# Kernel tuning notes

Measured on AMD Instinct MI355X. Metric: run time of the kernel, lower is better.

Reference implementation:

```python
import jax, jax.numpy as jnp
import numpy as np

B, S, H, HEAD = 4, 4096, 512, 128
GAMMA = 0.96875
SCALE_BASE = 512  # XPOS default scale_base


def rotate_every_two(x):
    # (..., d) -> interleave (-x2, x1) pairs, matching torch stack+flatten
    x1 = x[..., ::2]
    x2 = x[..., 1::2]
    return jnp.stack((-x2, x1), axis=-1).reshape(x.shape)


def duplicate_interleave(m):
    # (L, d/2) -> (L, d): each column repeated twice, interleaved
    return jnp.repeat(m, 2, axis=-1)


def xpos(x, downscale=False):
    # x: (B, L, d). Faithful to XPOS module with offset=0.
    L, d = x.shape[1], x.shape[2]
    half = d // 2
    base_scale = (jnp.arange(0, d, 2, dtype=jnp.float32) + 0.4 * d) / (1.4 * d)  # (half,)
    power = jnp.arange(L, dtype=jnp.float32)[:, None] / SCALE_BASE              # (L,1)
    scale = base_scale[None, :] ** power                                        # (L,half)
    inv_freq = 1.0 / (10000.0 ** (jnp.arange(half, dtype=jnp.float32) / half))  # (half,)
    sinusoid = jnp.arange(L, dtype=jnp.float32)[:, None] * inv_freq[None, :]    # (L,half)
    sin, cos = jnp.sin(sinusoid), jnp.cos(sinusoid)
    if downscale:
        scale = 1.0 / scale
    sin = duplicate_interleave(sin * scale)  # (L,d)
    cos = duplicate_interleave(cos * scale)  # (L,d)
    return x * cos[None] + rotate_every_two(x) * sin[None]


def decay_mask(s1, s2, gamma):
    n = jnp.arange(s1)[:, None]
    m = jnp.arange(s2)[None, :]
    keep = n >= m
    # guard exponent to avoid inf for n<m (original zeroes NaNs from inf*0)
    exp = jnp.where(keep, (n - m).astype(jnp.float32), 0.0)
    return jnp.where(keep, gamma ** exp, 0.0)  # (s1,s2)


def setup_inputs() -> dict:
    key = jax.random.key(0)
    k1, k2, k3, k4, k5 = jax.random.split(key, 5)
    return {
        "X": jax.random.normal(k1, (B, S, H), dtype=jnp.float32),
        "Mem": jax.random.normal(k2, (B, S, H), dtype=jnp.float32),
        "W_Q": jax.random.normal(k3, (H, HEAD), dtype=jnp.float32) / H,
        "W_K": jax.random.normal(k4, (H, HEAD), dtype=jnp.float32) / H,
        "W_V": jax.random.normal(k5, (H, HEAD), dtype=jnp.float32) / H,
    }


def reference(X, Mem, W_Q, W_K, W_V):
    s1, s2 = X.shape[1], Mem.shape[1]
    D = decay_mask(s1, s2, GAMMA)                 # (s1,s2)
    Q = xpos(X @ W_Q)                              # (B,s1,head)
    K = xpos(Mem @ W_K, downscale=True)            # (B,s2,head)
    V = Mem @ W_V                                  # (B,s2,v)
    ret = jnp.einsum("bnd,bmd->bnm", Q, K) * D[None]  # (B,s1,s2)
    return ret @ V                                 # (B,s1,v)
```

## Files before the change

### kernel.cpp

```cpp
#include <hip/hip_runtime.h>
#include <hip/hip_bf16.h>

#define S_LEN 4096
#define HID   512
#define HD    128
#define LOG2_GAMMA (-0.0458036933f)

typedef short bf16x8 __attribute__((ext_vector_type(8)));
typedef float f32x4  __attribute__((ext_vector_type(4)));
typedef unsigned short u16;

static __device__ __forceinline__ u16 f2bf(float f) {
    union { float f; unsigned u; } v; v.f = f;
    unsigned r = (v.u + 0x7fffu + ((v.u >> 16) & 1u)) >> 16;
    return (u16)r;
}

static __device__ __forceinline__ unsigned pk2(float lo, float hi) {
    __hip_bfloat162 h = __float22bfloat162_rn(make_float2(lo, hi));
    union { __hip_bfloat162 h; unsigned u; } c; c.h = h; return c.u;
}
static __device__ __forceinline__ bf16x8 pack8(float4 a, float4 b) {
    union { unsigned u[4]; bf16x8 v; } r;
    r.u[0] = pk2(a.x, a.y); r.u[1] = pk2(a.z, a.w);
    r.u[2] = pk2(b.x, b.y); r.u[3] = pk2(b.z, b.w);
    return r.v;
}

static __device__ __forceinline__ void gload16(const void* g, void* l) {
    __builtin_amdgcn_global_load_lds(
        (const __attribute__((address_space(1))) unsigned*)g,
        (__attribute__((address_space(3))) unsigned*)l, 16, 0, 0);
}

__global__ __launch_bounds__(256) void xpos_table_kernel(float2* __restrict__ tabQ,
                                                         float2* __restrict__ tabK) {
    int idx = blockIdx.x * 256 + threadIdx.x;
    int n = idx >> 6, i = idx & 63;
    float base  = (2.0f * i + 51.2f) * (1.0f / 179.2f);
    float power = (float)n * (1.0f / 512.0f);
    float scale = exp2f(power * log2f(base));
    float inv_freq = exp2f(-(float)i * (13.287712379549449f / 64.0f));
    float theta = (float)n * inv_freq;
    float s, c;
    sincosf(theta, &s, &c);
    tabQ[idx] = make_float2(c * scale, s * scale);
    float is = 1.0f / scale;
    tabK[idx] = make_float2(c * is, s * is);
}

__global__ __launch_bounds__(256) void wt_kernel(const float* __restrict__ WQ,
                                                 const float* __restrict__ WK,
                                                 const float* __restrict__ WV,
                                                 u16* __restrict__ Wt) {
    int idx = blockIdx.x * 256 + threadIdx.x;
    int w = idx >> 16;
    int rem = idx & 65535;
    int c = rem >> 9, k = rem & 511;
    const float* src = (w == 0) ? WQ : (w == 1) ? WK : WV;
    Wt[idx] = f2bf(src[k * HD + c]);
}

__global__ __launch_bounds__(256) void proj_kernel(const float* __restrict__ X,
                                                   const float* __restrict__ Mem,
                                                   const u16* __restrict__ Wt,
                                                   const float2* __restrict__ tabQ,
                                                   const float2* __restrict__ tabK,
                                                   u16* __restrict__ Qo,
                                                   u16* __restrict__ Ko,
                                                   u16* __restrict__ Vt) {
    __shared__ __align__(16) float A_lds[2][4096];
    __shared__ __align__(16) u16   B_lds[2][8192];
    const int which = blockIdx.y;
    const int tid  = threadIdx.x;
    const int wave = tid >> 6, lane = tid & 63;
    const int l15  = lane & 15, quad = lane >> 4;
    const int rt_base = blockIdx.x * 64;
    const float* src = (which == 0) ? X : Mem;
    const u16*  Wsel = Wt + which * 65536;

    auto stage = [&](int ch, int p) {
        const int kc0 = ch * 64;
#pragma unroll
        for (int i = 0; i < 4; ++i) {
            int u = i * 256 + tid;
            int row = u >> 4;
            int s = (u & 15) ^ (row & 15);
            gload16(src + (size_t)(rt_base + row) * HID + kc0 + s * 4,
                    &A_lds[p][(i * 256 + wave * 64) * 4]);
        }
#pragma unroll
        for (int i = 0; i < 4; ++i) {
            int u = i * 256 + tid;
            int col = u >> 3;
            int s = (u & 7) ^ (col & 7);
            gload16(Wsel + (size_t)col * HID + kc0 + s * 8,
                    &B_lds[p][(i * 256 + wave * 64) * 8]);
        }
    };

    f32x4 acc[8];
#pragma unroll
    for (int ct = 0; ct < 8; ++ct) acc[ct] = (f32x4){0.f, 0.f, 0.f, 0.f};

    stage(0, 0);
    for (int ch = 0; ch < 8; ++ch) {
        const int p = ch & 1;
        __syncthreads();
        if (ch < 7) stage(ch + 1, p ^ 1);
#pragma unroll
        for (int kc2 = 0; kc2 < 2; ++kc2) {
            const int s0 = kc2 * 8 + quad * 2;
            const int arow = wave * 16 + l15;
            float4 af0 = *(const float4*)&A_lds[p][(arow * 16 + ((s0    ) ^ l15)) * 4];
            float4 af1 = *(const float4*)&A_lds[p][(arow * 16 + ((s0 + 1) ^ l15)) * 4];
            bf16x8 a = pack8(af0, af1);
#pragma unroll
            for (int ct = 0; ct < 8; ++ct) {
                const int col = ct * 16 + l15;
                const int sb = (kc2 * 4 + quad) ^ (col & 7);
                bf16x8 bf = *(const bf16x8*)&B_lds[p][(col * 8 + sb) * 8];
                acc[ct] = __builtin_amdgcn_mfma_f32_16x16x32_bf16(a, bf, acc[ct], 0, 0, 0);
            }
        }
    }

    if (which <= 1) {
        const float2* tab = (which == 0) ? tabQ : tabK;
        u16* outp = (which == 0) ? Qo : Ko;
#pragma unroll
        for (int ct = 0; ct < 8; ++ct) {
            int j = ct * 16 + l15;
            int i = j >> 1;
            float sgn = (j & 1) ? 1.0f : -1.0f;
#pragma unroll
            for (int r = 0; r < 4; ++r) {
                int t = rt_base + wave * 16 + quad * 4 + r;
                int n = t & 4095;
                float2 cs = tab[n * 64 + i];
                float v = acc[ct][r];
                float partner = __shfl_xor(v, 1, 64);
                outp[(size_t)t * HD + j] = f2bf(v * cs.x + sgn * partner * cs.y);
            }
        }
    } else {
        u16* Vs = (u16*)&A_lds[0][0];
        __syncthreads();
#pragma unroll
        for (int ct = 0; ct < 8; ++ct) {
            int col = ct * 16 + l15;
#pragma unroll
            for (int r = 0; r < 4; ++r)
                Vs[col * 80 + wave * 16 + quad * 4 + r] = f2bf(acc[ct][r]);
        }
        __syncthreads();
        int b = rt_base >> 12, sb = rt_base & 4095;
        int h = tid >> 1, sof = (tid & 1) * 32;
#pragma unroll
        for (int pp = 0; pp < 4; ++pp) {
            bf16x8 v = *(const bf16x8*)&Vs[h * 80 + sof + pp * 8];
            *(bf16x8*)(Vt + (size_t)(b * 128 + h) * S_LEN + sb + sof + pp * 8) = v;
        }
    }
}

__global__ __launch_bounds__(256) void ret_kernel(const u16* __restrict__ Qb,
                                                  const u16* __restrict__ Kb,
                                                  const u16* __restrict__ Vt,
                                                  float* __restrict__ out) {
    __shared__ __align__(16) u16   K_lds[2][8192];
    __shared__ __align__(16) float P_lds[4][16][68];
    const int tid  = threadIdx.x;
    const int wave = tid >> 6, lane = tid & 63;
    const int l15  = lane & 15, quad = lane >> 4;
    const int b  = blockIdx.x >> 6;
    const int qt = (blockIdx.x & 63) * 64;
    const int qw = qt + wave * 16;

    auto stageK = [&](int kv0, int p) {
#pragma unroll
        for (int i = 0; i < 4; ++i) {
            int u = i * 256 + tid;
            int kvr = u >> 4;
            int s = (u & 15) ^ (kvr & 15);
            gload16(Kb + (size_t)(b * S_LEN + kv0 + kvr) * HD + s * 8,
                    &K_lds[p][(i * 256 + wave * 64) * 8]);
        }
    };

    const size_t tq = (size_t)(b * S_LEN + qw + l15);
    bf16x8 qfrag[4];
#pragma unroll
    for (int kc = 0; kc < 4; ++kc)
        qfrag[kc] = *(const bf16x8*)(Qb + tq * HD + kc * 32 + quad * 8);

    f32x4 acco[8];
#pragma unroll
    for (int ht = 0; ht < 8; ++ht) acco[ht] = (f32x4){0.f, 0.f, 0.f, 0.f};

    int kv_lo = qt - 448; if (kv_lo < 0) kv_lo = 0;
    const int nt = (qt + 64 - kv_lo) >> 6;

    stageK(kv_lo, 0);
    for (int it = 0; it < nt; ++it) {
        const int p = it & 1;
        const int kv0 = kv_lo + it * 64;
        __syncthreads();
        if (it + 1 < nt) stageK(kv0 + 64, p ^ 1);

        bf16x8 vf[8][2];
#pragma unroll
        for (int ht = 0; ht < 8; ++ht) {
            const u16* vb = Vt + (size_t)(b * HD + ht * 16 + l15) * S_LEN + kv0 + quad * 8;
            vf[ht][0] = *(const bf16x8*)vb;
            vf[ht][1] = *(const bf16x8*)(vb + 32);
        }

        f32x4 accs[4];
#pragma unroll
        for (int ct = 0; ct < 4; ++ct) accs[ct] = (f32x4){0.f, 0.f, 0.f, 0.f};
#pragma unroll
        for (int ct = 0; ct < 4; ++ct) {
            const int kvr = ct * 16 + l15;
#pragma unroll
            for (int kc = 0; kc < 4; ++kc) {
                bf16x8 kf = *(const bf16x8*)
                    &K_lds[p][(kvr * 16 + ((kc * 4 + quad) ^ (kvr & 15))) * 8];
                accs[ct] = __builtin_amdgcn_mfma_f32_16x16x32_bf16(qfrag[kc], kf, accs[ct], 0, 0, 0);
            }
        }
#pragma unroll
        for (int ct = 0; ct < 4; ++ct) {
            int kvi = kv0 + ct * 16 + l15;
#pragma unroll
            for (int r = 0; r < 4; ++r) {
                int d = (qw + quad * 4 + r) - kvi;
                float w = exp2f((float)d * LOG2_GAMMA);
                P_lds[wave][quad * 4 + r][ct * 16 + l15] = (d >= 0) ? accs[ct][r] * w : 0.0f;
            }
        }
        float4 p00 = *(const float4*)&P_lds[wave][l15][quad * 8];
        float4 p01 = *(const float4*)&P_lds[wave][l15][quad * 8 + 4];
        float4 p10 = *(const float4*)&P_lds[wave][l15][32 + quad * 8];
        float4 p11 = *(const float4*)&P_lds[wave][l15][32 + quad * 8 + 4];
        bf16x8 pa0 = pack8(p00, p01);
        bf16x8 pa1 = pack8(p10, p11);
#pragma unroll
        for (int ht = 0; ht < 8; ++ht) {
            acco[ht] = __builtin_amdgcn_mfma_f32_16x16x32_bf16(pa0, vf[ht][0], acco[ht], 0, 0, 0);
            acco[ht] = __builtin_amdgcn_mfma_f32_16x16x32_bf16(pa1, vf[ht][1], acco[ht], 0, 0, 0);
        }
    }

#pragma unroll
    for (int ht = 0; ht < 8; ++ht)
#pragma unroll
        for (int r = 0; r < 4; ++r)
            out[(size_t)(b * S_LEN + qw + quad * 4 + r) * HD + ht * 16 + l15] = acco[ht][r];
}

extern "C" void kernel_launch(void* const* d_in, const int* in_sizes, int n_in,
                              void* d_out, int out_size, void* d_ws, size_t ws_size,
                              hipStream_t stream) {
    const float* X   = (const float*)d_in[0];
    const float* Mem = (const float*)d_in[1];
    const float* WQ  = (const float*)d_in[2];
    const float* WK  = (const float*)d_in[3];
    const float* WV  = (const float*)d_in[4];
    float* out = (float*)d_out;

    char* ws = (char*)d_ws;
    u16*    Qb   = (u16*)(ws);
    u16*    Kb   = (u16*)(ws + ((size_t)4 << 20));
    u16*    Vt   = (u16*)(ws + ((size_t)8 << 20));
    u16*    Wt   = (u16*)(ws + ((size_t)12 << 20));
    float2* tabQ = (float2*)(ws + ((size_t)13 << 20));
    float2* tabK = (float2*)(ws + ((size_t)15 << 20));

    xpos_table_kernel<<<dim3(1024), dim3(256), 0, stream>>>(tabQ, tabK);
    wt_kernel<<<dim3(768), dim3(256), 0, stream>>>(WQ, WK, WV, Wt);
    proj_kernel<<<dim3(256, 3), dim3(256), 0, stream>>>(X, Mem, Wt, tabQ, tabK, Qb, Kb, Vt);
    ret_kernel<<<dim3(256), dim3(256), 0, stream>>>(Qb, Kb, Vt, out);
}
```

Measured before the change: 145.1 us.

## Split projection into Q and fused K/V kernels sharing Mem loads

The single projection kernel, launched as three grid slices (Q, K, V), is replaced by a Q kernel and a combined K/V kernel. The K/V kernel loads each Mem tile once and feeds it to both weight matrices, so Mem is read from global memory once instead of twice. The K-chunk per stage also shrinks from 64 to 32 with a new LDS swizzle, which cuts shared memory per block but doubles the number of stages and barriers. The two kernels now run back to back rather than in one 768-block grid, which may reduce overlap and occupancy per launch.

```diff
diff --git a/kernel.cpp b/kernel.cpp
--- a/kernel.cpp
+++ b/kernel.cpp
@@ -61,40 +61,33 @@
     Wt[idx] = f2bf(src[k * HD + c]);
 }
 
-__global__ __launch_bounds__(256) void proj_kernel(const float* __restrict__ X,
-                                                   const float* __restrict__ Mem,
-                                                   const u16* __restrict__ Wt,
-                                                   const float2* __restrict__ tabQ,
-                                                   const float2* __restrict__ tabK,
-                                                   u16* __restrict__ Qo,
-                                                   u16* __restrict__ Ko,
-                                                   u16* __restrict__ Vt) {
-    __shared__ __align__(16) float A_lds[2][4096];
-    __shared__ __align__(16) u16   B_lds[2][8192];
-    const int which = blockIdx.y;
+__global__ __launch_bounds__(256) void projQ_kernel(const float* __restrict__ X,
+                                                    const u16* __restrict__ Wt,
+                                                    const float2* __restrict__ tabQ,
+                                                    u16* __restrict__ Qo) {
+    __shared__ __align__(16) float A_lds[2][2048];
+    __shared__ __align__(16) u16   B_lds[2][4096];
     const int tid  = threadIdx.x;
     const int wave = tid >> 6, lane = tid & 63;
     const int l15  = lane & 15, quad = lane >> 4;
     const int rt_base = blockIdx.x * 64;
-    const float* src = (which == 0) ? X : Mem;
-    const u16*  Wsel = Wt + which * 65536;
 
     auto stage = [&](int ch, int p) {
-        const int kc0 = ch * 64;
-#pragma unroll
-        for (int i = 0; i < 4; ++i) {
-            int u = i * 256 + tid;
-            int row = u >> 4;
-            int s = (u & 15) ^ (row & 15);
-            gload16(src + (size_t)(rt_base + row) * HID + kc0 + s * 4,
+        const int kc0 = ch * 32;
+#pragma unroll
+        for (int i = 0; i < 2; ++i) {
+            int L = i * 256 + tid;
+            int row = L >> 3;
+            int s = (L & 7) ^ (row & 7);
+            gload16(X + (size_t)(rt_base + row) * HID + kc0 + s * 4,
                     &A_lds[p][(i * 256 + wave * 64) * 4]);
         }
 #pragma unroll
-        for (int i = 0; i < 4; ++i) {
-            int u = i * 256 + tid;
-            int col = u >> 3;
-            int s = (u & 7) ^ (col & 7);
-            gload16(Wsel + (size_t)col * HID + kc0 + s * 8,
+        for (int i = 0; i < 2; ++i) {
+            int L = i * 256 + tid;
+            int col = L >> 2;
+            int s = (L & 3) ^ ((col >> 1) & 3);
+            gload16(Wt + (size_t)col * HID + kc0 + s * 8,
                     &B_lds[p][(i * 256 + wave * 64) * 8]);
         }
     };
@@ -104,63 +97,139 @@
     for (int ct = 0; ct < 8; ++ct) acc[ct] = (f32x4){0.f, 0.f, 0.f, 0.f};
 
     stage(0, 0);
-    for (int ch = 0; ch < 8; ++ch) {
+    for (int ch = 0; ch < 16; ++ch) {
         const int p = ch & 1;
         __syncthreads();
-        if (ch < 7) stage(ch + 1, p ^ 1);
-#pragma unroll
-        for (int kc2 = 0; kc2 < 2; ++kc2) {
-            const int s0 = kc2 * 8 + quad * 2;
-            const int arow = wave * 16 + l15;
-            float4 af0 = *(const float4*)&A_lds[p][(arow * 16 + ((s0    ) ^ l15)) * 4];
-            float4 af1 = *(const float4*)&A_lds[p][(arow * 16 + ((s0 + 1) ^ l15)) * 4];
-            bf16x8 a = pack8(af0, af1);
-#pragma unroll
-            for (int ct = 0; ct < 8; ++ct) {
-                const int col = ct * 16 + l15;
-                const int sb = (kc2 * 4 + quad) ^ (col & 7);
-                bf16x8 bf = *(const bf16x8*)&B_lds[p][(col * 8 + sb) * 8];
-                acc[ct] = __builtin_amdgcn_mfma_f32_16x16x32_bf16(a, bf, acc[ct], 0, 0, 0);
-            }
-        }
-    }
-
-    if (which <= 1) {
-        const float2* tab = (which == 0) ? tabQ : tabK;
-        u16* outp = (which == 0) ? Qo : Ko;
+        if (ch < 15) stage(ch + 1, p ^ 1);
+        const int arow = wave * 16 + l15;
+        float4 af0 = *(const float4*)&A_lds[p][(arow * 8 + ((quad * 2    ) ^ (l15 & 7))) * 4];
+        float4 af1 = *(const float4*)&A_lds[p][(arow * 8 + ((quad * 2 + 1) ^ (l15 & 7))) * 4];
+        bf16x8 a = pack8(af0, af1);
 #pragma unroll
         for (int ct = 0; ct < 8; ++ct) {
-            int j = ct * 16 + l15;
-            int i = j >> 1;
-            float sgn = (j & 1) ? 1.0f : -1.0f;
-#pragma unroll
-            for (int r = 0; r < 4; ++r) {
-                int t = rt_base + wave * 16 + quad * 4 + r;
-                int n = t & 4095;
-                float2 cs = tab[n * 64 + i];
-                float v = acc[ct][r];
-                float partner = __shfl_xor(v, 1, 64);
-                outp[(size_t)t * HD + j] = f2bf(v * cs.x + sgn * partner * cs.y);
-            }
-        }
-    } else {
-        u16* Vs = (u16*)&A_lds[0][0];
+            const int bu = (ct * 16 + l15) * 4 + (quad ^ ((l15 >> 1) & 3));
+            bf16x8 b0 = *(const bf16x8*)&B_lds[p][bu * 8];
+            acc[ct] = __builtin_amdgcn_mfma_f32_16x16x32_bf16(a, b0, acc[ct], 0, 0, 0);
+        }
+    }
+
+#pragma unroll
+    for (int ct = 0; ct < 8; ++ct) {
+        int j = ct * 16 + l15;
+        int i = j >> 1;
+        float sgn = (j & 1) ? 1.0f : -1.0f;
+#pragma unroll
+        for (int r = 0; r < 4; ++r) {
+            int t = rt_base + wave * 16 + quad * 4 + r;
+            int n = t & 4095;
+            float2 cs = tabQ[n * 64 + i];
+            float v = acc[ct][r];
+            float partner = __shfl_xor(v, 1, 64);
+            Qo[(size_t)t * HD + j] = f2bf(v * cs.x + sgn * partner * cs.y);
+        }
+    }
+}
+
+__global__ __launch_bounds__(256) void projKV_kernel(const float* __restrict__ Mem,
+                                                     const u16* __restrict__ Wt,
+                                                     const float2* __restrict__ tabK,
+                                                     u16* __restrict__ Ko,
+                                                     u16* __restrict__ Vt) {
+    __shared__ __align__(16) float A_lds[2][2048];
+    __shared__ __align__(16) u16   B_lds[2][2][4096];
+    const int tid  = threadIdx.x;
+    const int wave = tid >> 6, lane = tid & 63;
+    const int l15  = lane & 15, quad = lane >> 4;
+    const int rt_base = blockIdx.x * 64;
+    const u16* WK_ = Wt + 65536;
+    const u16* WV_ = Wt + 131072;
+
+    auto stage = [&](int ch, int p) {
+        const int kc0 = ch * 32;
+#pragma unroll
+        for (int i = 0; i < 2; ++i) {
+            int L = i * 256 + tid;
+            int row = L >> 3;
+            int s = (L & 7) ^ (row & 7);
+            gload16(Mem + (size_t)(rt_base + row) * HID + kc0 + s * 4,
+                    &A_lds[p][(i * 256 + wave * 64) * 4]);
+        }
+#pragma unroll
+        for (int i = 0; i < 2; ++i) {
+            int L = i * 256 + tid;
+            int col = L >> 2;
+            int s = (L & 3) ^ ((col >> 1) & 3);
+            gload16(WK_ + (size_t)col * HID + kc0 + s * 8,
+                    &B_lds[p][0][(i * 256 + wave * 64) * 8]);
+        }
+#pragma unroll
+        for (int i = 0; i < 2; ++i) {
+            int L = i * 256 + tid;
+            int col = L >> 2;
+            int s = (L & 3) ^ ((col >> 1) & 3);
+            gload16(WV_ + (size_t)col * HID + kc0 + s * 8,
+                    &B_lds[p][1][(i * 256 + wave * 64) * 8]);
+        }
+    };
+
+    f32x4 acc0[8], acc1[8];
+#pragma unroll
+    for (int ct = 0; ct < 8; ++ct) {
+        acc0[ct] = (f32x4){0.f, 0.f, 0.f, 0.f};
+        acc1[ct] = (f32x4){0.f, 0.f, 0.f, 0.f};
+    }
+
+    stage(0, 0);
+    for (int ch = 0; ch < 16; ++ch) {
+        const int p = ch & 1;
         __syncthreads();
+        if (ch < 15) stage(ch + 1, p ^ 1);
+        const int arow = wave * 16 + l15;
+        float4 af0 = *(const float4*)&A_lds[p][(arow * 8 + ((quad * 2    ) ^ (l15 & 7))) * 4];
+        float4 af1 = *(const float4*)&A_lds[p][(arow * 8 + ((quad * 2 + 1) ^ (l15 & 7))) * 4];
+        bf16x8 a = pack8(af0, af1);
 #pragma unroll
         for (int ct = 0; ct < 8; ++ct) {
-            int col = ct * 16 + l15;
-#pragma unroll
-            for (int r = 0; r < 4; ++r)
-                Vs[col * 80 + wave * 16 + quad * 4 + r] = f2bf(acc[ct][r]);
-        }
-        __syncthreads();
-        int b = rt_base >> 12, sb = rt_base & 4095;
-        int h = tid >> 1, sof = (tid & 1) * 32;
-#pragma unroll
-        for (int pp = 0; pp < 4; ++pp) {
-            bf16x8 v = *(const bf16x8*)&Vs[h * 80 + sof + pp * 8];
-            *(bf16x8*)(Vt + (size_t)(b * 128 + h) * S_LEN + sb + sof + pp * 8) = v;
-        }
+            const int bu = (ct * 16 + l15) * 4 + (quad ^ ((l15 >> 1) & 3));
+            bf16x8 b0 = *(const bf16x8*)&B_lds[p][0][bu * 8];
+            bf16x8 b1 = *(const bf16x8*)&B_lds[p][1][bu * 8];
+            acc0[ct] = __builtin_amdgcn_mfma_f32_16x16x32_bf16(a, b0, acc0[ct], 0, 0, 0);
+            acc1[ct] = __builtin_amdgcn_mfma_f32_16x16x32_bf16(a, b1, acc1[ct], 0, 0, 0);
+        }
+    }
+
+#pragma unroll
+    for (int ct = 0; ct < 8; ++ct) {
+        int j = ct * 16 + l15;
+        int i = j >> 1;
+        float sgn = (j & 1) ? 1.0f : -1.0f;
+#pragma unroll
+        for (int r = 0; r < 4; ++r) {
+            int t = rt_base + wave * 16 + quad * 4 + r;
+            int n = t & 4095;
+            float2 cs = tabK[n * 64 + i];
+            float v = acc0[ct][r];
+            float partner = __shfl_xor(v, 1, 64);
+            Ko[(size_t)t * HD + j] = f2bf(v * cs.x + sgn * partner * cs.y);
+        }
+    }
+
+    u16* Vs = (u16*)&B_lds[0][0][0];
+    __syncthreads();
+#pragma unroll
+    for (int ct = 0; ct < 8; ++ct) {
+        int col = ct * 16 + l15;
+#pragma unroll
+        for (int r = 0; r < 4; ++r)
+            Vs[col * 80 + wave * 16 + quad * 4 + r] = f2bf(acc1[ct][r]);
+    }
+    __syncthreads();
+    int b = rt_base >> 12, sb = rt_base & 4095;
+    int h = tid >> 1, sof = (tid & 1) * 32;
+#pragma unroll
+    for (int pp = 0; pp < 4; ++pp) {
+        bf16x8 v = *(const bf16x8*)&Vs[h * 80 + sof + pp * 8];
+        *(bf16x8*)(Vt + (size_t)(b * 128 + h) * S_LEN + sb + sof + pp * 8) = v;
     }
 }
 
@@ -279,6 +348,7 @@
 
     xpos_table_kernel<<<dim3(1024), dim3(256), 0, stream>>>(tabQ, tabK);
     wt_kernel<<<dim3(768), dim3(256), 0, stream>>>(WQ, WK, WV, Wt);
-    proj_kernel<<<dim3(256, 3), dim3(256), 0, stream>>>(X, Mem, Wt, tabQ, tabK, Qb, Kb, Vt);
+    projQ_kernel<<<dim3(256), dim3(256), 0, stream>>>(X, Wt, tabQ, Qb);
+    projKV_kernel<<<dim3(256), dim3(256), 0, stream>>>(Mem, Wt, tabK, Kb, Vt);
     ret_kernel<<<dim3(256), dim3(256), 0, stream>>>(Qb, Kb, Vt, out);
 }
```

Result: slower. 165.0 us (+13.7%).

## Drop LDS staging; load MFMA fragments directly from global, fuse K and V projections

Applied to the files above, without the earlier changes.

The projection kernel no longer stages X/Mem and weight tiles through double-buffered LDS. Each wave now loads its A and B fragments straight from global memory with register prefetch. The K and V projections are merged into one block that reads Mem once and accumulates both outputs, so the grid shrinks from three row-groups to two. The retention kernel likewise drops LDS staging of K and its per-iteration barriers, loading K fragments from global/L2 per wave. This removes LDS traffic and syncs, at the cost of redundant global/L2 reads across waves, higher register pressure, and fewer blocks in flight.

```diff
diff --git a/kernel.cpp b/kernel.cpp
--- a/kernel.cpp
+++ b/kernel.cpp
@@ -25,12 +25,6 @@
     r.u[0] = pk2(a.x, a.y); r.u[1] = pk2(a.z, a.w);
     r.u[2] = pk2(b.x, b.y); r.u[3] = pk2(b.z, b.w);
     return r.v;
-}
-
-static __device__ __forceinline__ void gload16(const void* g, void* l) {
-    __builtin_amdgcn_global_load_lds(
-        (const __attribute__((address_space(1))) unsigned*)g,
-        (__attribute__((address_space(3))) unsigned*)l, 16, 0, 0);
 }
 
 __global__ __launch_bounds__(256) void xpos_table_kernel(float2* __restrict__ tabQ,
@@ -69,65 +63,46 @@
                                                    u16* __restrict__ Qo,
                                                    u16* __restrict__ Ko,
                                                    u16* __restrict__ Vt) {
-    __shared__ __align__(16) float A_lds[2][4096];
-    __shared__ __align__(16) u16   B_lds[2][8192];
-    const int which = blockIdx.y;
+    __shared__ u16 Vs[128 * 80];
     const int tid  = threadIdx.x;
     const int wave = tid >> 6, lane = tid & 63;
     const int l15  = lane & 15, quad = lane >> 4;
     const int rt_base = blockIdx.x * 64;
-    const float* src = (which == 0) ? X : Mem;
-    const u16*  Wsel = Wt + which * 65536;
-
-    auto stage = [&](int ch, int p) {
-        const int kc0 = ch * 64;
-#pragma unroll
-        for (int i = 0; i < 4; ++i) {
-            int u = i * 256 + tid;
-            int row = u >> 4;
-            int s = (u & 15) ^ (row & 15);
-            gload16(src + (size_t)(rt_base + row) * HID + kc0 + s * 4,
-                    &A_lds[p][(i * 256 + wave * 64) * 4]);
-        }
-#pragma unroll
-        for (int i = 0; i < 4; ++i) {
-            int u = i * 256 + tid;
-            int col = u >> 3;
-            int s = (u & 7) ^ (col & 7);
-            gload16(Wsel + (size_t)col * HID + kc0 + s * 8,
-                    &B_lds[p][(i * 256 + wave * 64) * 8]);
-        }
-    };
-
-    f32x4 acc[8];
-#pragma unroll
-    for (int ct = 0; ct < 8; ++ct) acc[ct] = (f32x4){0.f, 0.f, 0.f, 0.f};
-
-    stage(0, 0);
-    for (int ch = 0; ch < 8; ++ch) {
-        const int p = ch & 1;
-        __syncthreads();
-        if (ch < 7) stage(ch + 1, p ^ 1);
-#pragma unroll
-        for (int kc2 = 0; kc2 < 2; ++kc2) {
-            const int s0 = kc2 * 8 + quad * 2;
-            const int arow = wave * 16 + l15;
-            float4 af0 = *(const float4*)&A_lds[p][(arow * 16 + ((s0    ) ^ l15)) * 4];
-            float4 af1 = *(const float4*)&A_lds[p][(arow * 16 + ((s0 + 1) ^ l15)) * 4];
-            bf16x8 a = pack8(af0, af1);
-#pragma unroll
-            for (int ct = 0; ct < 8; ++ct) {
-                const int col = ct * 16 + l15;
-                const int sb = (kc2 * 4 + quad) ^ (col & 7);
-                bf16x8 bf = *(const bf16x8*)&B_lds[p][(col * 8 + sb) * 8];
-                acc[ct] = __builtin_amdgcn_mfma_f32_16x16x32_bf16(a, bf, acc[ct], 0, 0, 0);
-            }
-        }
-    }
-
-    if (which <= 1) {
-        const float2* tab = (which == 0) ? tabQ : tabK;
-        u16* outp = (which == 0) ? Qo : Ko;
+
+    if (blockIdx.y == 0) {
+        const float* arow = X + (size_t)(rt_base + wave * 16 + l15) * HID + quad * 8;
+        const u16*   bb   = Wt + (size_t)l15 * HID + quad * 8;
+
+        f32x4 acc[8];
+#pragma unroll
+        for (int ct = 0; ct < 8; ++ct) acc[ct] = (f32x4){0.f, 0.f, 0.f, 0.f};
+
+        float4 a0 = *(const float4*)arow;
+        float4 a1 = *(const float4*)(arow + 4);
+        bf16x8 bc[8];
+#pragma unroll
+        for (int ct = 0; ct < 8; ++ct) bc[ct] = *(const bf16x8*)(bb + ct * 16 * HID);
+
+        for (int ch = 0; ch < 16; ++ch) {
+            float4 an0, an1; bf16x8 bn[8];
+            if (ch < 15) {
+                an0 = *(const float4*)(arow + (ch + 1) * 32);
+                an1 = *(const float4*)(arow + (ch + 1) * 32 + 4);
+#pragma unroll
+                for (int ct = 0; ct < 8; ++ct)
+                    bn[ct] = *(const bf16x8*)(bb + ct * 16 * HID + (ch + 1) * 32);
+            }
+            bf16x8 a = pack8(a0, a1);
+#pragma unroll
+            for (int ct = 0; ct < 8; ++ct)
+                acc[ct] = __builtin_amdgcn_mfma_f32_16x16x32_bf16(a, bc[ct], acc[ct], 0, 0, 0);
+            if (ch < 15) {
+                a0 = an0; a1 = an1;
+#pragma unroll
+                for (int ct = 0; ct < 8; ++ct) bc[ct] = bn[ct];
+            }
+        }
+
 #pragma unroll
         for (int ct = 0; ct < 8; ++ct) {
             int j = ct * 16 + l15;
@@ -137,21 +112,79 @@
             for (int r = 0; r < 4; ++r) {
                 int t = rt_base + wave * 16 + quad * 4 + r;
                 int n = t & 4095;
-                float2 cs = tab[n * 64 + i];
+                float2 cs = tabQ[n * 64 + i];
                 float v = acc[ct][r];
                 float partner = __shfl_xor(v, 1, 64);
-                outp[(size_t)t * HD + j] = f2bf(v * cs.x + sgn * partner * cs.y);
+                Qo[(size_t)t * HD + j] = f2bf(v * cs.x + sgn * partner * cs.y);
             }
         }
     } else {
-        u16* Vs = (u16*)&A_lds[0][0];
-        __syncthreads();
+        const float* arow = Mem + (size_t)(rt_base + wave * 16 + l15) * HID + quad * 8;
+        const u16*   bbK  = Wt + 65536  + (size_t)l15 * HID + quad * 8;
+        const u16*   bbV  = Wt + 131072 + (size_t)l15 * HID + quad * 8;
+
+        f32x4 acc0[8], acc1[8];
+#pragma unroll
+        for (int ct = 0; ct < 8; ++ct) {
+            acc0[ct] = (f32x4){0.f, 0.f, 0.f, 0.f};
+            acc1[ct] = (f32x4){0.f, 0.f, 0.f, 0.f};
+        }
+
+        float4 a0 = *(const float4*)arow;
+        float4 a1 = *(const float4*)(arow + 4);
+        bf16x8 bcK[8], bcV[8];
+#pragma unroll
+        for (int ct = 0; ct < 8; ++ct) {
+            bcK[ct] = *(const bf16x8*)(bbK + ct * 16 * HID);
+            bcV[ct] = *(const bf16x8*)(bbV + ct * 16 * HID);
+        }
+
+        for (int ch = 0; ch < 16; ++ch) {
+            float4 an0, an1; bf16x8 bnK[8], bnV[8];
+            if (ch < 15) {
+                an0 = *(const float4*)(arow + (ch + 1) * 32);
+                an1 = *(const float4*)(arow + (ch + 1) * 32 + 4);
+#pragma unroll
+                for (int ct = 0; ct < 8; ++ct) {
+                    bnK[ct] = *(const bf16x8*)(bbK + ct * 16 * HID + (ch + 1) * 32);
+                    bnV[ct] = *(const bf16x8*)(bbV + ct * 16 * HID + (ch + 1) * 32);
+                }
+            }
+            bf16x8 a = pack8(a0, a1);
+#pragma unroll
+            for (int ct = 0; ct < 8; ++ct) {
+                acc0[ct] = __builtin_amdgcn_mfma_f32_16x16x32_bf16(a, bcK[ct], acc0[ct], 0, 0, 0);
+                acc1[ct] = __builtin_amdgcn_mfma_f32_16x16x32_bf16(a, bcV[ct], acc1[ct], 0, 0, 0);
+            }
+            if (ch < 15) {
+                a0 = an0; a1 = an1;
+#pragma unroll
+                for (int ct = 0; ct < 8; ++ct) { bcK[ct] = bnK[ct]; bcV[ct] = bnV[ct]; }
+            }
+        }
+
+#pragma unroll
+        for (int ct = 0; ct < 8; ++ct) {
+            int j = ct * 16 + l15;
+            int i = j >> 1;
+            float sgn = (j & 1) ? 1.0f : -1.0f;
+#pragma unroll
+            for (int r = 0; r < 4; ++r) {
+                int t = rt_base + wave * 16 + quad * 4 + r;
+                int n = t & 4095;
+                float2 cs = tabK[n * 64 + i];
+                float v = acc0[ct][r];
+                float partner = __shfl_xor(v, 1, 64);
+                Ko[(size_t)t * HD + j] = f2bf(v * cs.x + sgn * partner * cs.y);
+            }
+        }
+
 #pragma unroll
         for (int ct = 0; ct < 8; ++ct) {
             int col = ct * 16 + l15;
 #pragma unroll
             for (int r = 0; r < 4; ++r)
-                Vs[col * 80 + wave * 16 + quad * 4 + r] = f2bf(acc[ct][r]);
+                Vs[col * 80 + wave * 16 + quad * 4 + r] = f2bf(acc1[ct][r]);
         }
         __syncthreads();
         int b = rt_base >> 12, sb = rt_base & 4095;
@@ -168,7 +201,6 @@
                                                   const u16* __restrict__ Kb,
                                                   const u16* __restrict__ Vt,
                                                   float* __restrict__ out) {
-    __shared__ __align__(16) u16   K_lds[2][8192];
     __shared__ __align__(16) float P_lds[4][16][68];
     const int tid  = threadIdx.x;
     const int wave = tid >> 6, lane = tid & 63;
@@ -177,17 +209,6 @@
     const int qt = (blockIdx.x & 63) * 64;
     const int qw = qt + wave * 16;
 
-    auto stageK = [&](int kv0, int p) {
-#pragma unroll
-        for (int i = 0; i < 4; ++i) {
-            int u = i * 256 + tid;
-            int kvr = u >> 4;
-            int s = (u & 15) ^ (kvr & 15);
-            gload16(Kb + (size_t)(b * S_LEN + kv0 + kvr) * HD + s * 8,
-                    &K_lds[p][(i * 256 + wave * 64) * 8]);
-        }
-    };
-
     const size_t tq = (size_t)(b * S_LEN + qw + l15);
     bf16x8 qfrag[4];
 #pragma unroll
@@ -201,13 +222,17 @@
     int kv_lo = qt - 448; if (kv_lo < 0) kv_lo = 0;
     const int nt = (qt + 64 - kv_lo) >> 6;
 
-    stageK(kv_lo, 0);
     for (int it = 0; it < nt; ++it) {
-        const int p = it & 1;
         const int kv0 = kv_lo + it * 64;
-        __syncthreads();
-        if (it + 1 < nt) stageK(kv0 + 64, p ^ 1);
-
+
+        bf16x8 kf[4][4];
+#pragma unroll
+        for (int ct = 0; ct < 4; ++ct) {
+            const u16* kb = Kb + (size_t)(b * S_LEN + kv0 + ct * 16 + l15) * HD + quad * 8;
+#pragma unroll
+            for (int kc = 0; kc < 4; ++kc)
+                kf[ct][kc] = *(const bf16x8*)(kb + kc * 32);
+        }
         bf16x8 vf[8][2];
 #pragma unroll
         for (int ht = 0; ht < 8; ++ht) {
@@ -220,15 +245,11 @@
 #pragma unroll
         for (int ct = 0; ct < 4; ++ct) accs[ct] = (f32x4){0.f, 0.f, 0.f, 0.f};
 #pragma unroll
-        for (int ct = 0; ct < 4; ++ct) {
-            const int kvr = ct * 16 + l15;
-#pragma unroll
-            for (int kc = 0; kc < 4; ++kc) {
-                bf16x8 kf = *(const bf16x8*)
-                    &K_lds[p][(kvr * 16 + ((kc * 4 + quad) ^ (kvr & 15))) * 8];
-                accs[ct] = __builtin_amdgcn_mfma_f32_16x16x32_bf16(qfrag[kc], kf, accs[ct], 0, 0, 0);
-            }
-        }
+        for (int ct = 0; ct < 4; ++ct)
+#pragma unroll
+            for (int kc = 0; kc < 4; ++kc)
+                accs[ct] = __builtin_amdgcn_mfma_f32_16x16x32_bf16(qfrag[kc], kf[ct][kc], accs[ct], 0, 0, 0);
+
 #pragma unroll
         for (int ct = 0; ct < 4; ++ct) {
             int kvi = kv0 + ct * 16 + l15;
@@ -279,6 +300,6 @@
 
     xpos_table_kernel<<<dim3(1024), dim3(256), 0, stream>>>(tabQ, tabK);
     wt_kernel<<<dim3(768), dim3(256), 0, stream>>>(WQ, WK, WV, Wt);
-    proj_kernel<<<dim3(256, 3), dim3(256), 0, stream>>>(X, Mem, Wt, tabQ, tabK, Qb, Kb, Vt);
+    proj_kernel<<<dim3(256, 2), dim3(256), 0, stream>>>(X, Mem, Wt, tabQ, tabK, Qb, Kb, Vt);
     ret_kernel<<<dim3(256), dim3(256), 0, stream>>>(Qb, Kb, Vt, out);
 }
```

Result: slower. 191.6 us (+32.0%).

## Split projection and retention kernels into single-wave blocks and merge prep kernels

Applied to the files above, without the earlier changes.

The two setup kernels (xpos table and weight transpose) are merged into one launch. The projection kernel now uses one 64-lane wave per block, split over 32-column groups, and computes K and V together from a shared Mem tile. The retention kernel now uses one wave per 16-query-row block with a tighter, 16-row-granular key range. Both kernels drop `__syncthreads` in favour of an unrolled two-buffer prefetch loop. This adds parallel blocks and cuts launch overhead, at the cost of re-reading X/Mem and K tiles across more blocks. It also relies on in-wave ordering of async global-to-LDS loads with no explicit barriers.

```diff
diff --git a/kernel.cpp b/kernel.cpp
--- a/kernel.cpp
+++ b/kernel.cpp
@@ -33,158 +33,178 @@
         (__attribute__((address_space(3))) unsigned*)l, 16, 0, 0);
 }
 
-__global__ __launch_bounds__(256) void xpos_table_kernel(float2* __restrict__ tabQ,
-                                                         float2* __restrict__ tabK) {
-    int idx = blockIdx.x * 256 + threadIdx.x;
-    int n = idx >> 6, i = idx & 63;
-    float base  = (2.0f * i + 51.2f) * (1.0f / 179.2f);
-    float power = (float)n * (1.0f / 512.0f);
-    float scale = exp2f(power * log2f(base));
-    float inv_freq = exp2f(-(float)i * (13.287712379549449f / 64.0f));
-    float theta = (float)n * inv_freq;
-    float s, c;
-    sincosf(theta, &s, &c);
-    tabQ[idx] = make_float2(c * scale, s * scale);
-    float is = 1.0f / scale;
-    tabK[idx] = make_float2(c * is, s * is);
-}
-
-__global__ __launch_bounds__(256) void wt_kernel(const float* __restrict__ WQ,
-                                                 const float* __restrict__ WK,
-                                                 const float* __restrict__ WV,
-                                                 u16* __restrict__ Wt) {
-    int idx = blockIdx.x * 256 + threadIdx.x;
-    int w = idx >> 16;
-    int rem = idx & 65535;
-    int c = rem >> 9, k = rem & 511;
-    const float* src = (w == 0) ? WQ : (w == 1) ? WK : WV;
-    Wt[idx] = f2bf(src[k * HD + c]);
-}
-
-__global__ __launch_bounds__(256) void proj_kernel(const float* __restrict__ X,
-                                                   const float* __restrict__ Mem,
-                                                   const u16* __restrict__ Wt,
-                                                   const float2* __restrict__ tabQ,
-                                                   const float2* __restrict__ tabK,
-                                                   u16* __restrict__ Qo,
-                                                   u16* __restrict__ Ko,
-                                                   u16* __restrict__ Vt) {
-    __shared__ __align__(16) float A_lds[2][4096];
-    __shared__ __align__(16) u16   B_lds[2][8192];
-    const int which = blockIdx.y;
-    const int tid  = threadIdx.x;
-    const int wave = tid >> 6, lane = tid & 63;
+__global__ __launch_bounds__(256) void prep_kernel(const float* __restrict__ WQ,
+                                                   const float* __restrict__ WK,
+                                                   const float* __restrict__ WV,
+                                                   u16* __restrict__ Wt,
+                                                   float2* __restrict__ tabQ,
+                                                   float2* __restrict__ tabK) {
+    if (blockIdx.x < 1024) {
+        int idx = blockIdx.x * 256 + threadIdx.x;
+        int n = idx >> 6, i = idx & 63;
+        float base  = (2.0f * i + 51.2f) * (1.0f / 179.2f);
+        float power = (float)n * (1.0f / 512.0f);
+        float scale = exp2f(power * log2f(base));
+        float inv_freq = exp2f(-(float)i * (13.287712379549449f / 64.0f));
+        float theta = (float)n * inv_freq;
+        float s, c;
+        sincosf(theta, &s, &c);
+        tabQ[idx] = make_float2(c * scale, s * scale);
+        float is = 1.0f / scale;
+        tabK[idx] = make_float2(c * is, s * is);
+    } else {
+        int idx = (blockIdx.x - 1024) * 256 + threadIdx.x;
+        int w = idx >> 16;
+        int rem = idx & 65535;
+        int c = rem >> 9, k = rem & 511;
+        const float* src = (w == 0) ? WQ : (w == 1) ? WK : WV;
+        Wt[idx] = f2bf(src[k * HD + c]);
+    }
+}
+
+__global__ __launch_bounds__(64) void proj_kernel(const float* __restrict__ X,
+                                                  const float* __restrict__ Mem,
+                                                  const u16* __restrict__ Wt,
+                                                  const float2* __restrict__ tabQ,
+                                                  const float2* __restrict__ tabK,
+                                                  u16* __restrict__ Qo,
+                                                  u16* __restrict__ Ko,
+                                                  u16* __restrict__ Vt) {
+    __shared__ __align__(16) float A_lds[2][2048];
+    __shared__ __align__(16) u16   B_lds[2][2][1024];
+    const int lane = threadIdx.x;
     const int l15  = lane & 15, quad = lane >> 4;
     const int rt_base = blockIdx.x * 64;
-    const float* src = (which == 0) ? X : Mem;
-    const u16*  Wsel = Wt + which * 65536;
-
-    auto stage = [&](int ch, int p) {
-        const int kc0 = ch * 64;
-#pragma unroll
-        for (int i = 0; i < 4; ++i) {
-            int u = i * 256 + tid;
-            int row = u >> 4;
-            int s = (u & 15) ^ (row & 15);
+    const bool isQ = (blockIdx.y < 4);
+    const int cg = blockIdx.y & 3;
+    const float* src = isQ ? X : Mem;
+    const u16* W0 = isQ ? Wt : (Wt + 65536);
+    const u16* W1 = Wt + 131072;
+
+    auto stageA = [&](int ch, int p) {
+        const int kc0 = ch * 32;
+#pragma unroll
+        for (int i = 0; i < 8; ++i) {
+            int L = i * 64 + lane;
+            int row = L >> 3;
+            int s = (L & 7) ^ (row & 7);
             gload16(src + (size_t)(rt_base + row) * HID + kc0 + s * 4,
-                    &A_lds[p][(i * 256 + wave * 64) * 4]);
-        }
-#pragma unroll
-        for (int i = 0; i < 4; ++i) {
-            int u = i * 256 + tid;
-            int col = u >> 3;
-            int s = (u & 7) ^ (col & 7);
-            gload16(Wsel + (size_t)col * HID + kc0 + s * 8,
-                    &B_lds[p][(i * 256 + wave * 64) * 8]);
-        }
-    };
-
-    f32x4 acc[8];
-#pragma unroll
-    for (int ct = 0; ct < 8; ++ct) acc[ct] = (f32x4){0.f, 0.f, 0.f, 0.f};
-
-    stage(0, 0);
-    for (int ch = 0; ch < 8; ++ch) {
-        const int p = ch & 1;
-        __syncthreads();
-        if (ch < 7) stage(ch + 1, p ^ 1);
-#pragma unroll
-        for (int kc2 = 0; kc2 < 2; ++kc2) {
-            const int s0 = kc2 * 8 + quad * 2;
-            const int arow = wave * 16 + l15;
-            float4 af0 = *(const float4*)&A_lds[p][(arow * 16 + ((s0    ) ^ l15)) * 4];
-            float4 af1 = *(const float4*)&A_lds[p][(arow * 16 + ((s0 + 1) ^ l15)) * 4];
+                    &A_lds[p][i * 256]);
+        }
+    };
+    auto stageB = [&](const u16* W, int m, int ch, int p) {
+        const int kc0 = ch * 32;
+#pragma unroll
+        for (int i = 0; i < 2; ++i) {
+            int L = i * 64 + lane;
+            int col = L >> 2;
+            int s = (L & 3) ^ ((col >> 1) & 3);
+            gload16(W + (size_t)(cg * 32 + col) * HID + kc0 + s * 8,
+                    &B_lds[p][m][i * 512]);
+        }
+    };
+
+    f32x4 acc0[4][2], acc1[4][2];
+#pragma unroll
+    for (int rt = 0; rt < 4; ++rt)
+#pragma unroll
+        for (int ct = 0; ct < 2; ++ct) {
+            acc0[rt][ct] = (f32x4){0.f, 0.f, 0.f, 0.f};
+            acc1[rt][ct] = (f32x4){0.f, 0.f, 0.f, 0.f};
+        }
+
+    auto compute = [&](int p) {
+#pragma unroll
+        for (int rt = 0; rt < 4; ++rt) {
+            const int ar = rt * 16 + l15;
+            float4 af0 = *(const float4*)&A_lds[p][(ar * 8 + ((quad * 2    ) ^ (ar & 7))) * 4];
+            float4 af1 = *(const float4*)&A_lds[p][(ar * 8 + ((quad * 2 + 1) ^ (ar & 7))) * 4];
             bf16x8 a = pack8(af0, af1);
 #pragma unroll
-            for (int ct = 0; ct < 8; ++ct) {
-                const int col = ct * 16 + l15;
-                const int sb = (kc2 * 4 + quad) ^ (col & 7);
-                bf16x8 bf = *(const bf16x8*)&B_lds[p][(col * 8 + sb) * 8];
-                acc[ct] = __builtin_amdgcn_mfma_f32_16x16x32_bf16(a, bf, acc[ct], 0, 0, 0);
+            for (int ct = 0; ct < 2; ++ct) {
+                const int bu = (ct * 16 + l15) * 4 + (quad ^ ((l15 >> 1) & 3));
+                bf16x8 b0 = *(const bf16x8*)&B_lds[p][0][bu * 8];
+                acc0[rt][ct] = __builtin_amdgcn_mfma_f32_16x16x32_bf16(a, b0, acc0[rt][ct], 0, 0, 0);
+                if (!isQ) {
+                    bf16x8 b1 = *(const bf16x8*)&B_lds[p][1][bu * 8];
+                    acc1[rt][ct] = __builtin_amdgcn_mfma_f32_16x16x32_bf16(a, b1, acc1[rt][ct], 0, 0, 0);
+                }
             }
         }
-    }
-
-    if (which <= 1) {
-        const float2* tab = (which == 0) ? tabQ : tabK;
-        u16* outp = (which == 0) ? Qo : Ko;
-#pragma unroll
-        for (int ct = 0; ct < 8; ++ct) {
-            int j = ct * 16 + l15;
+    };
+
+    stageA(0, 0); stageB(W0, 0, 0, 0); if (!isQ) stageB(W1, 1, 0, 0);
+    for (int ch = 0; ch < 16; ch += 2) {
+        if (ch + 1 < 16) { stageA(ch + 1, 1); stageB(W0, 0, ch + 1, 1); if (!isQ) stageB(W1, 1, ch + 1, 1); }
+        compute(0);
+        if (ch + 2 < 16) { stageA(ch + 2, 0); stageB(W0, 0, ch + 2, 0); if (!isQ) stageB(W1, 1, ch + 2, 0); }
+        if (ch + 1 < 16) compute(1);
+    }
+
+    {
+        const float2* tab = isQ ? tabQ : tabK;
+        u16* outp = isQ ? Qo : Ko;
+#pragma unroll
+        for (int ct = 0; ct < 2; ++ct) {
+            int j = cg * 32 + ct * 16 + l15;
             int i = j >> 1;
             float sgn = (j & 1) ? 1.0f : -1.0f;
 #pragma unroll
-            for (int r = 0; r < 4; ++r) {
-                int t = rt_base + wave * 16 + quad * 4 + r;
-                int n = t & 4095;
-                float2 cs = tab[n * 64 + i];
-                float v = acc[ct][r];
-                float partner = __shfl_xor(v, 1, 64);
-                outp[(size_t)t * HD + j] = f2bf(v * cs.x + sgn * partner * cs.y);
+            for (int rt = 0; rt < 4; ++rt) {
+#pragma unroll
+                for (int r = 0; r < 4; ++r) {
+                    int t = rt_base + rt * 16 + quad * 4 + r;
+                    int n = t & 4095;
+                    float2 cs = tab[n * 64 + i];
+                    float v = acc0[rt][ct][r];
+                    float partner = __shfl_xor(v, 1, 64);
+                    outp[(size_t)t * HD + j] = f2bf(v * cs.x + sgn * partner * cs.y);
+                }
             }
         }
-    } else {
+    }
+
+    if (!isQ) {
         u16* Vs = (u16*)&A_lds[0][0];
-        __syncthreads();
-#pragma unroll
-        for (int ct = 0; ct < 8; ++ct) {
-            int col = ct * 16 + l15;
-#pragma unroll
-            for (int r = 0; r < 4; ++r)
-                Vs[col * 80 + wave * 16 + quad * 4 + r] = f2bf(acc[ct][r]);
-        }
-        __syncthreads();
+#pragma unroll
+        for (int ct = 0; ct < 2; ++ct) {
+            int cl = ct * 16 + l15;
+#pragma unroll
+            for (int rt = 0; rt < 4; ++rt)
+#pragma unroll
+                for (int r = 0; r < 4; ++r)
+                    Vs[cl * 72 + rt * 16 + quad * 4 + r] = f2bf(acc1[rt][ct][r]);
+        }
         int b = rt_base >> 12, sb = rt_base & 4095;
-        int h = tid >> 1, sof = (tid & 1) * 32;
+        int hl = lane >> 1, sof = (lane & 1) * 32;
+        int h = cg * 32 + hl;
 #pragma unroll
         for (int pp = 0; pp < 4; ++pp) {
-            bf16x8 v = *(const bf16x8*)&Vs[h * 80 + sof + pp * 8];
+            bf16x8 v = *(const bf16x8*)&Vs[hl * 72 + sof + pp * 8];
             *(bf16x8*)(Vt + (size_t)(b * 128 + h) * S_LEN + sb + sof + pp * 8) = v;
         }
     }
 }
 
-__global__ __launch_bounds__(256) void ret_kernel(const u16* __restrict__ Qb,
-                                                  const u16* __restrict__ Kb,
-                                                  const u16* __restrict__ Vt,
-                                                  float* __restrict__ out) {
+__global__ __launch_bounds__(64) void ret_kernel(const u16* __restrict__ Qb,
+                                                 const u16* __restrict__ Kb,
+                                                 const u16* __restrict__ Vt,
+                                                 float* __restrict__ out) {
     __shared__ __align__(16) u16   K_lds[2][8192];
-    __shared__ __align__(16) float P_lds[4][16][68];
-    const int tid  = threadIdx.x;
-    const int wave = tid >> 6, lane = tid & 63;
+    __shared__ __align__(16) float P_lds[16][68];
+    const int lane = threadIdx.x;
     const int l15  = lane & 15, quad = lane >> 4;
-    const int b  = blockIdx.x >> 6;
-    const int qt = (blockIdx.x & 63) * 64;
-    const int qw = qt + wave * 16;
+    const int b  = blockIdx.x >> 8;
+    const int qw = (blockIdx.x & 255) * 16;
 
     auto stageK = [&](int kv0, int p) {
 #pragma unroll
-        for (int i = 0; i < 4; ++i) {
-            int u = i * 256 + tid;
-            int kvr = u >> 4;
-            int s = (u & 15) ^ (kvr & 15);
+        for (int i = 0; i < 16; ++i) {
+            int L = i * 64 + lane;
+            int kvr = L >> 4;
+            int s = (L & 15) ^ (kvr & 15);
             gload16(Kb + (size_t)(b * S_LEN + kv0 + kvr) * HD + s * 8,
-                    &K_lds[p][(i * 256 + wave * 64) * 8]);
+                    &K_lds[p][i * 512]);
         }
     };
 
@@ -198,16 +218,12 @@
 #pragma unroll
     for (int ht = 0; ht < 8; ++ht) acco[ht] = (f32x4){0.f, 0.f, 0.f, 0.f};
 
-    int kv_lo = qt - 448; if (kv_lo < 0) kv_lo = 0;
-    const int nt = (qt + 64 - kv_lo) >> 6;
-
-    stageK(kv_lo, 0);
-    for (int it = 0; it < nt; ++it) {
-        const int p = it & 1;
+    int kv_lo = (qw - 448) & ~63;
+    if (kv_lo < 0) kv_lo = 0;
+    const int nt = (qw + 16 - kv_lo + 63) >> 6;
+
+    auto tile = [&](int it, int p) {
         const int kv0 = kv_lo + it * 64;
-        __syncthreads();
-        if (it + 1 < nt) stageK(kv0 + 64, p ^ 1);
-
         bf16x8 vf[8][2];
 #pragma unroll
         for (int ht = 0; ht < 8; ++ht) {
@@ -215,7 +231,6 @@
             vf[ht][0] = *(const bf16x8*)vb;
             vf[ht][1] = *(const bf16x8*)(vb + 32);
         }
-
         f32x4 accs[4];
 #pragma unroll
         for (int ct = 0; ct < 4; ++ct) accs[ct] = (f32x4){0.f, 0.f, 0.f, 0.f};
@@ -236,13 +251,13 @@
             for (int r = 0; r < 4; ++r) {
                 int d = (qw + quad * 4 + r) - kvi;
                 float w = exp2f((float)d * LOG2_GAMMA);
-                P_lds[wave][quad * 4 + r][ct * 16 + l15] = (d >= 0) ? accs[ct][r] * w : 0.0f;
+                P_lds[quad * 4 + r][ct * 16 + l15] = (d >= 0) ? accs[ct][r] * w : 0.0f;
             }
         }
-        float4 p00 = *(const float4*)&P_lds[wave][l15][quad * 8];
-        float4 p01 = *(const float4*)&P_lds[wave][l15][quad * 8 + 4];
-        float4 p10 = *(const float4*)&P_lds[wave][l15][32 + quad * 8];
-        float4 p11 = *(const float4*)&P_lds[wave][l15][32 + quad * 8 + 4];
+        float4 p00 = *(const float4*)&P_lds[l15][quad * 8];
+        float4 p01 = *(const float4*)&P_lds[l15][quad * 8 + 4];
+        float4 p10 = *(const float4*)&P_lds[l15][32 + quad * 8];
+        float4 p11 = *(const float4*)&P_lds[l15][32 + quad * 8 + 4];
         bf16x8 pa0 = pack8(p00, p01);
         bf16x8 pa1 = pack8(p10, p11);
 #pragma unroll
@@ -250,6 +265,14 @@
             acco[ht] = __builtin_amdgcn_mfma_f32_16x16x32_bf16(pa0, vf[ht][0], acco[ht], 0, 0, 0);
             acco[ht] = __builtin_amdgcn_mfma_f32_16x16x32_bf16(pa1, vf[ht][1], acco[ht], 0, 0, 0);
         }
+    };
+
+    stageK(kv_lo, 0);
+    for (int it = 0; it < nt; it += 2) {
+        if (it + 1 < nt) stageK(kv_lo + (it + 1) * 64, 1);
+        tile(it, 0);
+        if (it + 2 < nt) stageK(kv_lo + (it + 2) * 64, 0);
+        if (it + 1 < nt) tile(it + 1, 1);
     }
 
 #pragma unroll
@@ -277,8 +300,7 @@
     float2* tabQ = (float2*)(ws + ((size_t)13 << 20));
     float2* tabK = (float2*)(ws + ((size_t)15 << 20));
 
-    xpos_table_kernel<<<dim3(1024), dim3(256), 0, stream>>>(tabQ, tabK);
-    wt_kernel<<<dim3(768), dim3(256), 0, stream>>>(WQ, WK, WV, Wt);
-    proj_kernel<<<dim3(256, 3), dim3(256), 0, stream>>>(X, Mem, Wt, tabQ, tabK, Qb, Kb, Vt);
-    ret_kernel<<<dim3(256), dim3(256), 0, stream>>>(Qb, Kb, Vt, out);
-}
+    prep_kernel<<<dim3(1792), dim3(256), 0, stream>>>(WQ, WK, WV, Wt, tabQ, tabK);
+    proj_kernel<<<dim3(256, 8), dim3(64), 0, stream>>>(X, Mem, Wt, tabQ, tabK, Qb, Kb, Vt);
+    ret_kernel<<<dim3(1024), dim3(64), 0, stream>>>(Qb, Kb, Vt, out);
+}
```

Result: slower. 168.3 us (+16.0%).
